# Performance work log

Hardware: AMD Instinct MI355X
Metric: run time of the kernel (lower is better)

The kernel has to match this reference:

```python
import jax, jax.numpy as jnp
import numpy as np

NUM_TOKENS = 1024  # codebook size (n_embed)
CODE_DIM = 256     # embedding_dim
BETA = 0.25


def setup_inputs() -> dict:
    key = jax.random.key(0)
    k1, k2 = jax.random.split(key)
    z = jax.random.normal(k1, (64, 512, CODE_DIM), dtype=jnp.float32)
    weight = jax.random.normal(k2, (NUM_TOKENS, CODE_DIM), dtype=jnp.float32)
    return {"z": z, "weight": weight}


def reference(z, weight):
    # z: [B, T, D]; weight: [K, D]
    z_flat = z.reshape(-1, CODE_DIM)                       # [N, D]
    # squared euclidean distances: ||z||^2 + ||w||^2 - 2 z.w
    d = (jnp.sum(z_flat ** 2, axis=1, keepdims=True)
         + jnp.sum(weight ** 2, axis=1)
         - 2.0 * jnp.matmul(z_flat, weight.T))             # [N, K]
    min_encoding_indices = jnp.argmin(d, axis=1)           # [N]
    z_q = weight[min_encoding_indices].reshape(z.shape)    # gather

    # perplexity from mean one-hot usage (avoid materializing one-hot via bincount)
    counts = jnp.bincount(min_encoding_indices, length=NUM_TOKENS)
    e_mean = counts.astype(z.dtype) / z_flat.shape[0]
    perplexity = jnp.exp(-jnp.sum(e_mean * jnp.log(e_mean + 1e-10)))

    # commitment loss (codebook is EMA-updated, so z_q is detached)
    loss = BETA * jnp.mean((jax.lax.stop_gradient(z_q) - z) ** 2)
    # straight-through estimator
    z_q_st = z + jax.lax.stop_gradient(z_q - z)
    return (loss, z_q_st, min_encoding_indices, perplexity)
```

## Files before the change

kernel.cpp:

```cpp
#include <hip/hip_runtime.h>

#define N_TOKENS 32768
#define K_CODES  1024
#define DIM      256
#define BETA     0.25f

typedef unsigned long long u64;
typedef _Float16 half8 __attribute__((ext_vector_type(8)));
typedef float floatx4 __attribute__((ext_vector_type(4)));

__global__ void init_kernel(const float* __restrict__ w, float* __restrict__ wn,
                            int* __restrict__ counts, u64* __restrict__ keys) {
    int k = blockIdx.x;
    int lane = threadIdx.x;
    float4 v = *(const float4*)(w + (size_t)k * DIM + lane * 4);
    float s = v.x * v.x + v.y * v.y + v.z * v.z + v.w * v.w;
    #pragma unroll
    for (int off = 32; off; off >>= 1) s += __shfl_down(s, off);
    if (lane == 0) { wn[k] = s; counts[k] = 0; }
    if (lane < 32) keys[k * 32 + lane] = ~0ull;
}

__global__ __launch_bounds__(256, 2) void argmin_kernel(
    const float* __restrict__ z, const float* __restrict__ w,
    const float* __restrict__ wn, u64* __restrict__ keys)
{
    constexpr int ZS = 40;
    __shared__ _Float16 zhi[128 * ZS], zlo[128 * ZS];
    __shared__ _Float16 whi[128 * ZS], wlo[128 * ZS];
    __shared__ float wns[128];

    const int tid  = threadIdx.x;
    const int lane = tid & 63;
    const int wid  = tid >> 6;
    const int wm   = wid >> 1;
    const int wq   = wid & 1;
    const int t_   = blockIdx.x & 255;
    const int q    = blockIdx.x >> 8;
    const int tok0  = t_ * 128;
    const int kbase = q * 128;

    if (tid < 128) wns[tid] = wn[kbase + tid];

    floatx4 acc[4][4];
    #pragma unroll
    for (int i = 0; i < 4; i++)
        #pragma unroll
        for (int j = 0; j < 4; j++)
            acc[i][j] = (floatx4){0.f, 0.f, 0.f, 0.f};

    const int r0 = tid >> 2;
    const int g0 = tid & 3;

    for (int dt = 0; dt < 8; ++dt) {
        const int d0 = dt * 32;
        __syncthreads();

        #pragma unroll
        for (int s = 0; s < 2; s++) {
            int t = r0 + s * 64;
            const float* p = z + (size_t)(tok0 + t) * DIM + d0 + g0 * 8;
            float4 a = *(const float4*)p;
            float4 b = *(const float4*)(p + 4);
            float vals[8] = {a.x, a.y, a.z, a.w, b.x, b.y, b.z, b.w};
            half8 hv, lv;
            #pragma unroll
            for (int e = 0; e < 8; e++) {
                _Float16 h = (_Float16)vals[e];
                hv[e] = h;
                lv[e] = (_Float16)(vals[e] - (float)h);
            }
            *(half8*)&zhi[t * ZS + g0 * 8] = hv;
            *(half8*)&zlo[t * ZS + g0 * 8] = lv;
        }
        #pragma unroll
        for (int s = 0; s < 2; s++) {
            int t = r0 + s * 64;
            const float* p = w + (size_t)(kbase + t) * DIM + d0 + g0 * 8;
            float4 a = *(const float4*)p;
            float4 b = *(const float4*)(p + 4);
            float vals[8] = {a.x, a.y, a.z, a.w, b.x, b.y, b.z, b.w};
            half8 hv, lv;
            #pragma unroll
            for (int e = 0; e < 8; e++) {
                _Float16 h = (_Float16)vals[e];
                hv[e] = h;
                lv[e] = (_Float16)(vals[e] - (float)h);
            }
            *(half8*)&whi[t * ZS + g0 * 8] = hv;
            *(half8*)&wlo[t * ZS + g0 * 8] = lv;
        }
        __syncthreads();

        half8 ah[4], al[4], bh[4], bl[4];
        const int koff = (lane >> 4) * 8;
        #pragma unroll
        for (int i = 0; i < 4; i++) {
            int za_off = (wm * 64 + i * 16 + (lane & 15)) * ZS + koff;
            ah[i] = *(const half8*)&zhi[za_off];
            al[i] = *(const half8*)&zlo[za_off];
            int wb_off = (wq * 64 + i * 16 + (lane & 15)) * ZS + koff;
            bh[i] = *(const half8*)&whi[wb_off];
            bl[i] = *(const half8*)&wlo[wb_off];
        }
        #pragma unroll
        for (int i = 0; i < 4; i++)
            #pragma unroll
            for (int j = 0; j < 4; j++) {
                acc[i][j] = __builtin_amdgcn_mfma_f32_16x16x32_f16(ah[i], bh[j], acc[i][j], 0, 0, 0);
                acc[i][j] = __builtin_amdgcn_mfma_f32_16x16x32_f16(ah[i], bl[j], acc[i][j], 0, 0, 0);
                acc[i][j] = __builtin_amdgcn_mfma_f32_16x16x32_f16(al[i], bh[j], acc[i][j], 0, 0, 0);
            }
    }

    #pragma unroll
    for (int i = 0; i < 4; i++) {
        #pragma unroll
        for (int r = 0; r < 4; r++) {
            float bv = 3.4e38f; int bi = 0;
            #pragma unroll
            for (int j = 0; j < 4; j++) {
                int cl = wq * 64 + j * 16 + (lane & 15);
                float dist = wns[cl] - 2.0f * acc[i][j][r];
                if (dist < bv) { bv = dist; bi = kbase + cl; }
            }
            unsigned uu = __float_as_uint(bv);
            unsigned ss = (uu & 0x80000000u) ? ~uu : (uu | 0x80000000u);
            u64 key = ((u64)ss << 32) | (unsigned)bi;
            #pragma unroll
            for (int m = 1; m < 16; m <<= 1) {
                u64 o = __shfl_xor(key, m);
                if (o < key) key = o;
            }
            if ((lane & 15) == 0) {
                int token = tok0 + wm * 64 + i * 16 + (lane >> 4) * 4 + r;
                atomicMin(&keys[token], key);
            }
        }
    }
}

__global__ void gather_loss_kernel(const float* __restrict__ z,
                                   const float* __restrict__ w,
                                   const u64* __restrict__ keys,
                                   float* __restrict__ zq_out,
                                   float* __restrict__ idxf,
                                   int* __restrict__ counts,
                                   float* __restrict__ partials)
{
    __shared__ float red[4];
    int tid = threadIdx.x;
    int lane = tid & 63;
    int wid = blockIdx.x * 4 + (tid >> 6);
    float s = 0.0f;
    #pragma unroll
    for (int it = 0; it < 4; it++) {
        int tok = wid + it * 8192;
        u64 key = 0;
        if (lane == 0) key = keys[tok];
        key = __shfl(key, 0);
        int k = (int)(unsigned)(key & 0xFFFFFFFFull);
        float4 wv = *(const float4*)(w + (size_t)k * DIM + lane * 4);
        float4 zv = *(const float4*)(z + (size_t)tok * DIM + lane * 4);
        *(float4*)(zq_out + (size_t)tok * DIM + lane * 4) = wv;
        float dx = wv.x - zv.x, dy = wv.y - zv.y, dz = wv.z - zv.z, dw = wv.w - zv.w;
        s += dx * dx + dy * dy + dz * dz + dw * dw;
        if (lane == 0) {
            idxf[tok] = (float)k;
            atomicAdd(&counts[k], 1);
        }
    }
    #pragma unroll
    for (int off = 32; off; off >>= 1) s += __shfl_down(s, off);
    if (lane == 0) red[tid >> 6] = s;
    __syncthreads();
    if (tid == 0)
        partials[blockIdx.x] = red[0] + red[1] + red[2] + red[3];
}

__global__ void finalize_kernel(const int* __restrict__ counts,
                                const float* __restrict__ partials,
                                float* __restrict__ loss_out,
                                float* __restrict__ ppl_out)
{
    __shared__ float redE[16], redL[16];
    int tid = threadIdx.x;
    float e = (float)counts[tid] * (1.0f / (float)N_TOKENS);
    float t = -e * logf(e + 1e-10f);
    float p = partials[tid] + partials[tid + 1024];
    #pragma unroll
    for (int off = 32; off; off >>= 1) {
        t += __shfl_down(t, off);
        p += __shfl_down(p, off);
    }
    if ((tid & 63) == 0) { redE[tid >> 6] = t; redL[tid >> 6] = p; }
    __syncthreads();
    if (tid == 0) {
        float se = 0.0f, sl = 0.0f;
        #pragma unroll
        for (int i = 0; i < 16; i++) { se += redE[i]; sl += redL[i]; }
        *ppl_out = expf(se);
        *loss_out = BETA * sl / (float)((size_t)N_TOKENS * DIM);
    }
}

extern "C" void kernel_launch(void* const* d_in, const int* in_sizes, int n_in,
                              void* d_out, int out_size, void* d_ws, size_t ws_size,
                              hipStream_t stream) {
    const float* z = (const float*)d_in[0];
    const float* w = (const float*)d_in[1];
    float* out = (float*)d_out;

    float* loss_out = out;
    float* zq_out   = out + 1;
    float* idxf     = out + 1 + (size_t)N_TOKENS * DIM;
    float* ppl_out  = out + (out_size - 1);

    float* wn       = (float*)d_ws;
    int*   counts   = (int*)d_ws + 1024;
    float* partials = (float*)d_ws + 2048;
    u64*   keys     = (u64*)((char*)d_ws + 16384);

    init_kernel<<<K_CODES, 64, 0, stream>>>(w, wn, counts, keys);
    argmin_kernel<<<8 * 256, 256, 0, stream>>>(z, w, wn, keys);
    gather_loss_kernel<<<2048, 256, 0, stream>>>(z, w, keys, zq_out, idxf, counts, partials);
    finalize_kernel<<<1, 1024, 0, stream>>>(counts, partials, loss_out, ppl_out);
}
```

Baseline: 170.7 us.

## Precompute fp16 hi/lo codebook split and widen argmin tile to 256 codes

The init kernel now writes the fp16 hi/lo split of the codebook to workspace once, so the argmin kernel loads ready-made halves instead of converting fp32 weights in every block. The argmin tile grows from 128 to 256 codes per block, halving the grid and the number of times each z tile is loaded and split. In exchange, accumulator registers per thread double (128 floats), shared memory grows, and occupancy may drop under the 2-blocks launch bound.

New measurement: 159.1 us. -6.8%, faster.

```diff
diff --git a/kernel.cpp b/kernel.cpp
--- a/kernel.cpp
+++ b/kernel.cpp
@@ -10,11 +10,20 @@
 typedef float floatx4 __attribute__((ext_vector_type(4)));
 
 __global__ void init_kernel(const float* __restrict__ w, float* __restrict__ wn,
-                            int* __restrict__ counts, u64* __restrict__ keys) {
+                            int* __restrict__ counts, u64* __restrict__ keys,
+                            _Float16* __restrict__ whiG, _Float16* __restrict__ wloG) {
     int k = blockIdx.x;
     int lane = threadIdx.x;
     float4 v = *(const float4*)(w + (size_t)k * DIM + lane * 4);
-    float s = v.x * v.x + v.y * v.y + v.z * v.z + v.w * v.w;
+    float vals[4] = {v.x, v.y, v.z, v.w};
+    float s = 0.f;
+    #pragma unroll
+    for (int e = 0; e < 4; e++) {
+        s += vals[e] * vals[e];
+        _Float16 h = (_Float16)vals[e];
+        whiG[k * DIM + lane * 4 + e] = h;
+        wloG[k * DIM + lane * 4 + e] = (_Float16)(vals[e] - (float)h);
+    }
     #pragma unroll
     for (int off = 32; off; off >>= 1) s += __shfl_down(s, off);
     if (lane == 0) { wn[k] = s; counts[k] = 0; }
@@ -22,13 +31,14 @@
 }
 
 __global__ __launch_bounds__(256, 2) void argmin_kernel(
-    const float* __restrict__ z, const float* __restrict__ w,
-    const float* __restrict__ wn, u64* __restrict__ keys)
+    const float* __restrict__ z, const _Float16* __restrict__ whiG,
+    const _Float16* __restrict__ wloG, const float* __restrict__ wn,
+    u64* __restrict__ keys)
 {
     constexpr int ZS = 40;
     __shared__ _Float16 zhi[128 * ZS], zlo[128 * ZS];
-    __shared__ _Float16 whi[128 * ZS], wlo[128 * ZS];
-    __shared__ float wns[128];
+    __shared__ _Float16 whi[256 * ZS], wlo[256 * ZS];
+    __shared__ float wns[256];
 
     const int tid  = threadIdx.x;
     const int lane = tid & 63;
@@ -38,15 +48,15 @@
     const int t_   = blockIdx.x & 255;
     const int q    = blockIdx.x >> 8;
     const int tok0  = t_ * 128;
-    const int kbase = q * 128;
-
-    if (tid < 128) wns[tid] = wn[kbase + tid];
-
-    floatx4 acc[4][4];
+    const int kbase = q * 256;
+
+    wns[tid] = wn[kbase + tid];
+
+    floatx4 acc[4][8];
     #pragma unroll
     for (int i = 0; i < 4; i++)
         #pragma unroll
-        for (int j = 0; j < 4; j++)
+        for (int j = 0; j < 8; j++)
             acc[i][j] = (floatx4){0.f, 0.f, 0.f, 0.f};
 
     const int r0 = tid >> 2;
@@ -74,43 +84,34 @@
             *(half8*)&zlo[t * ZS + g0 * 8] = lv;
         }
         #pragma unroll
-        for (int s = 0; s < 2; s++) {
+        for (int s = 0; s < 4; s++) {
             int t = r0 + s * 64;
-            const float* p = w + (size_t)(kbase + t) * DIM + d0 + g0 * 8;
-            float4 a = *(const float4*)p;
-            float4 b = *(const float4*)(p + 4);
-            float vals[8] = {a.x, a.y, a.z, a.w, b.x, b.y, b.z, b.w};
-            half8 hv, lv;
-            #pragma unroll
-            for (int e = 0; e < 8; e++) {
-                _Float16 h = (_Float16)vals[e];
-                hv[e] = h;
-                lv[e] = (_Float16)(vals[e] - (float)h);
-            }
-            *(half8*)&whi[t * ZS + g0 * 8] = hv;
-            *(half8*)&wlo[t * ZS + g0 * 8] = lv;
+            size_t goff = (size_t)(kbase + t) * DIM + d0 + g0 * 8;
+            *(half8*)&whi[t * ZS + g0 * 8] = *(const half8*)&whiG[goff];
+            *(half8*)&wlo[t * ZS + g0 * 8] = *(const half8*)&wloG[goff];
         }
         __syncthreads();
 
-        half8 ah[4], al[4], bh[4], bl[4];
         const int koff = (lane >> 4) * 8;
+        half8 ah[4], al[4];
         #pragma unroll
         for (int i = 0; i < 4; i++) {
-            int za_off = (wm * 64 + i * 16 + (lane & 15)) * ZS + koff;
-            ah[i] = *(const half8*)&zhi[za_off];
-            al[i] = *(const half8*)&zlo[za_off];
-            int wb_off = (wq * 64 + i * 16 + (lane & 15)) * ZS + koff;
-            bh[i] = *(const half8*)&whi[wb_off];
-            bl[i] = *(const half8*)&wlo[wb_off];
-        }
-        #pragma unroll
-        for (int i = 0; i < 4; i++)
-            #pragma unroll
-            for (int j = 0; j < 4; j++) {
-                acc[i][j] = __builtin_amdgcn_mfma_f32_16x16x32_f16(ah[i], bh[j], acc[i][j], 0, 0, 0);
-                acc[i][j] = __builtin_amdgcn_mfma_f32_16x16x32_f16(ah[i], bl[j], acc[i][j], 0, 0, 0);
-                acc[i][j] = __builtin_amdgcn_mfma_f32_16x16x32_f16(al[i], bh[j], acc[i][j], 0, 0, 0);
-            }
+            int off = (wm * 64 + i * 16 + (lane & 15)) * ZS + koff;
+            ah[i] = *(const half8*)&zhi[off];
+            al[i] = *(const half8*)&zlo[off];
+        }
+        #pragma unroll
+        for (int j = 0; j < 8; j++) {
+            int off = (wq * 128 + j * 16 + (lane & 15)) * ZS + koff;
+            half8 bh = *(const half8*)&whi[off];
+            half8 bl = *(const half8*)&wlo[off];
+            #pragma unroll
+            for (int i = 0; i < 4; i++) {
+                acc[i][j] = __builtin_amdgcn_mfma_f32_16x16x32_f16(ah[i], bh, acc[i][j], 0, 0, 0);
+                acc[i][j] = __builtin_amdgcn_mfma_f32_16x16x32_f16(ah[i], bl, acc[i][j], 0, 0, 0);
+                acc[i][j] = __builtin_amdgcn_mfma_f32_16x16x32_f16(al[i], bh, acc[i][j], 0, 0, 0);
+            }
+        }
     }
 
     #pragma unroll
@@ -119,8 +120,8 @@
         for (int r = 0; r < 4; r++) {
             float bv = 3.4e38f; int bi = 0;
             #pragma unroll
-            for (int j = 0; j < 4; j++) {
-                int cl = wq * 64 + j * 16 + (lane & 15);
+            for (int j = 0; j < 8; j++) {
+                int cl = wq * 128 + j * 16 + (lane & 15);
                 float dist = wns[cl] - 2.0f * acc[i][j][r];
                 if (dist < bv) { bv = dist; bi = kbase + cl; }
             }
@@ -220,9 +221,11 @@
     int*   counts   = (int*)d_ws + 1024;
     float* partials = (float*)d_ws + 2048;
     u64*   keys     = (u64*)((char*)d_ws + 16384);
-
-    init_kernel<<<K_CODES, 64, 0, stream>>>(w, wn, counts, keys);
-    argmin_kernel<<<8 * 256, 256, 0, stream>>>(z, w, wn, keys);
+    _Float16* whiG  = (_Float16*)((char*)d_ws + 16384 + (size_t)N_TOKENS * 8);
+    _Float16* wloG  = whiG + (size_t)K_CODES * DIM;
+
+    init_kernel<<<K_CODES, 64, 0, stream>>>(w, wn, counts, keys, whiG, wloG);
+    argmin_kernel<<<4 * 256, 256, 0, stream>>>(z, whiG, wloG, wn, keys);
     gather_loss_kernel<<<2048, 256, 0, stream>>>(z, w, keys, zq_out, idxf, counts, partials);
     finalize_kernel<<<1, 1024, 0, stream>>>(counts, partials, loss_out, ppl_out);
 }
```
